# Performance work log

Measured on AMD Instinct MI355X. Metric: run time of the kernel, lower is better.

## Reference

```python
import jax, jax.numpy as jnp
import numpy as np

B, S, D_MODEL, H = 2, 2048, 1024, 16
DK = D_MODEL // H
THETA = 10000.0


def setup_inputs() -> dict:
    key = jax.random.key(0)
    ks = jax.random.split(key, 5)
    scale = 0.02  # keep logits in a numerically sane range
    return {
        "x": jax.random.normal(ks[0], (B, S, D_MODEL), jnp.float32),
        "Q_weight": jax.random.normal(ks[1], (D_MODEL, D_MODEL), jnp.float32) * scale,
        "K_weight": jax.random.normal(ks[2], (D_MODEL, D_MODEL), jnp.float32) * scale,
        "V_weight": jax.random.normal(ks[3], (D_MODEL, D_MODEL), jnp.float32) * scale,
        "O_weight": jax.random.normal(ks[4], (D_MODEL, D_MODEL), jnp.float32) * scale,
        "token_positions": jnp.arange(S, dtype=jnp.int32),
    }


def _rope(x, token_positions, theta, d_k):
    # x: [..., seq, d_k]; rotate interleaved even/odd pairs
    inv_freq = 1.0 / theta ** (jnp.arange(0, d_k, 2, dtype=jnp.float32) / d_k)
    ang = token_positions.astype(jnp.float32)[:, None] * inv_freq  # [S, d_k/2]
    cos, sin = jnp.cos(ang), jnp.sin(ang)
    x0, x1 = x[..., 0::2], x[..., 1::2]
    y0 = x0 * cos - x1 * sin
    y1 = x0 * sin + x1 * cos
    return jnp.stack([y0, y1], axis=-1).reshape(x.shape)


def _mhsa(x, Qw, Kw, Vw, Ow, token_positions):
    b, s, d = x.shape
    qw = Qw.reshape(H, DK, d)
    kw = Kw.reshape(H, DK, d)
    vw = Vw.reshape(H, DK, d)
    q = jnp.einsum('hki,bsi->bhsk', qw, x)
    k = jnp.einsum('hki,bsi->bhsk', kw, x)
    v = jnp.einsum('hvi,bsi->bhsv', vw, x)
    q = _rope(q, token_positions, THETA, DK)
    k = _rope(k, token_positions, THETA, DK)
    scores = jnp.einsum('bhnd,bhmd->bhnm', q, k) / jnp.sqrt(jnp.float32(DK))
    causal = jnp.tril(jnp.ones((s, s), dtype=bool))
    scores = jnp.where(causal, scores, -jnp.inf)
    attn = jax.nn.softmax(scores, axis=-1)
    o = jnp.einsum('bhnm,bhmv->bhnv', attn, v)  # [B,H,S,DV]
    o = jnp.transpose(o, (0, 2, 1, 3)).reshape(b, s, H * DK)
    return jnp.einsum('dv,bsv->bsd', Ow, o)


def reference(x, Q_weight, K_weight, V_weight, O_weight, token_positions):
    return _mhsa(x, Q_weight, K_weight, V_weight, O_weight, token_positions)
```

## Files before the change

kernel.cpp:

```cpp
#include <hip/hip_runtime.h>

#define NB 2
#define NS 2048
#define NDM 1024
#define NH 16
#define NDK 64

typedef unsigned int u32;
typedef u32 u32x4 __attribute__((ext_vector_type(4)));
typedef float f32x4 __attribute__((ext_vector_type(4)));
typedef float f32x2 __attribute__((ext_vector_type(2)));
typedef __bf16 bf16x8 __attribute__((ext_vector_type(8)));
typedef __bf16 bf16x4 __attribute__((ext_vector_type(4)));
typedef __bf16 bf16x2 __attribute__((ext_vector_type(2)));

#define QSCALE 0.18033688011112042f
#define EXP2F(x) __builtin_amdgcn_exp2f(x)

__device__ __forceinline__ void gload_lds16(const __bf16* g, __bf16* l) {
    __builtin_amdgcn_global_load_lds(
        (const __attribute__((address_space(1))) unsigned int*)(g),
        (__attribute__((address_space(3))) unsigned int*)(l), 16, 0, 0);
}

__global__ __launch_bounds__(256) void cvt_all(const float* __restrict__ x,
                                               const float* __restrict__ qw,
                                               const float* __restrict__ kw,
                                               const float* __restrict__ vw,
                                               const float* __restrict__ ow,
                                               const int* __restrict__ tp,
                                               __bf16* __restrict__ xb,
                                               __bf16* __restrict__ wqkv,
                                               __bf16* __restrict__ owb,
                                               float* __restrict__ tbl) {
    const int i = blockIdx.x * 256 + threadIdx.x;
    if (i >= 2097152) {
        const int it = i - 2097152;
        if (it < NS * 32) {
            const int s = it >> 5, jj = it & 31;
            const float pos = (float)tp[s];
            const float inv = exp2f(-0.41524101186092f * (float)jj);
            const float ang = pos * inv;
            float sn, cs;
            sincosf(ang, &sn, &cs);
            f32x2 o; o[0] = cs; o[1] = sn;
            *(f32x2*)&tbl[(size_t)it * 2] = o;
        }
        return;
    }
    const float* src;
    __bf16* dst;
    if (i < 1048576) {
        src = x + (size_t)i * 4;
        dst = xb + (size_t)i * 4;
    } else {
        const int j = i - 1048576;
        const int seg = j >> 18;
        const int off = j & 0x3FFFF;
        src = ((seg == 0) ? qw : (seg == 1) ? kw : (seg == 2) ? vw : ow) + (size_t)off * 4;
        if (seg <= 1) {
            const int row = off >> 8;
            const int c4 = off & 255;
            const int h = row >> 6, fr = row & 63;
            const int pr = (fr >> 1) | ((fr & 1) << 5);
            dst = wqkv + (((size_t)(seg << 10) + h * 64 + pr) << 10) + (size_t)c4 * 4;
        } else {
            dst = ((seg == 3) ? owb : wqkv + (size_t)seg * 1048576) + (size_t)off * 4;
        }
    }
    f32x4 v = *(const f32x4*)src;
    bf16x4 o;
    o[0] = (__bf16)v[0]; o[1] = (__bf16)v[1]; o[2] = (__bf16)v[2]; o[3] = (__bf16)v[3];
    *(bf16x4*)dst = o;
}

__global__ __launch_bounds__(256) void gemm_qkv128(const __bf16* __restrict__ A,
                                                   const __bf16* __restrict__ Bt,
                                                   const float* __restrict__ tbl,
                                                   __bf16* __restrict__ Qr,
                                                   __bf16* __restrict__ Kr,
                                                   __bf16* __restrict__ Vt) {
    __shared__ __bf16 As[2][128 * 64];
    __shared__ __bf16 Bs[2][128 * 64];
    const int K = 1024, lda = 1024, ldb = 1024;
    const int tid = threadIdx.x;
    const int lane = tid & 63, w = tid >> 6;
    const int wr = w >> 1, wc = w & 1;
    const int l15 = lane & 15, lg = lane >> 4;
    const int m0 = blockIdx.y * 128, n0 = blockIdx.x * 128;
    const int crow = lane >> 3;
    const int csw = ((lane & 7) ^ crow) * 8;

    f32x4 acc[4][4];
    const f32x4 z = {0.f, 0.f, 0.f, 0.f};
#pragma unroll
    for (int i = 0; i < 4; ++i)
#pragma unroll
        for (int jx = 0; jx < 4; ++jx) acc[i][jx] = z;

    auto stage = [&](int buf, int k0) {
#pragma unroll
        for (int ch = 0; ch < 4; ++ch) {
            const int cid = w * 4 + ch;
            const int ra = cid * 8 + crow;
            gload_lds16(&A[(size_t)(m0 + ra) * lda + k0 + csw], &As[buf][cid * 512]);
            gload_lds16(&Bt[(size_t)(n0 + ra) * ldb + k0 + csw], &Bs[buf][cid * 512]);
        }
    };

    stage(0, 0);
    int cur = 0;
    for (int k0 = 0; k0 < K; k0 += 64) {
        if (k0 + 64 < K) {
            stage(cur ^ 1, k0 + 64);
            asm volatile("s_waitcnt vmcnt(8)" ::: "memory");
        } else {
            asm volatile("s_waitcnt vmcnt(0)" ::: "memory");
        }
        __builtin_amdgcn_s_barrier();
        __builtin_amdgcn_sched_barrier(0);
#pragma unroll
        for (int kc = 0; kc < 2; ++kc) {
            bf16x8 af[4], bfv[4];
#pragma unroll
            for (int i = 0; i < 4; ++i) {
                const int ra = wr * 64 + i * 16 + l15;
                const int rb = wc * 64 + i * 16 + l15;
                af[i]  = *(const bf16x8*)&As[cur][ra * 64 + ((kc * 32 + lg * 8) ^ ((ra & 7) << 3))];
                bfv[i] = *(const bf16x8*)&Bs[cur][rb * 64 + ((kc * 32 + lg * 8) ^ ((rb & 7) << 3))];
            }
#pragma unroll
            for (int sm = 0; sm < 4; ++sm)
#pragma unroll
                for (int sn = 0; sn < 4; ++sn)
                    acc[sm][sn] = __builtin_amdgcn_mfma_f32_16x16x32_bf16(af[sm], bfv[sn], acc[sm][sn], 0, 0, 0);
        }
        asm volatile("s_waitcnt lgkmcnt(0)" ::: "memory");
        __builtin_amdgcn_s_barrier();
        __builtin_amdgcn_sched_barrier(0);
        cur ^= 1;
    }
    if (n0 < 2048) {
        __bf16* dst = (n0 < 1024) ? Qr : Kr;
        const float scale = (n0 < 1024) ? QSCALE : 1.0f;
        const int h = ((n0 & 1023) + wc * 64) >> 6;
#pragma unroll
        for (int sm = 0; sm < 4; ++sm)
#pragma unroll
            for (int j = 0; j < 4; ++j) {
                const int row = m0 + wr * 64 + sm * 16 + lg * 4 + j;
                const int b = row >> 11, s = row & (NS - 1);
                const size_t base = ((size_t)(b * NH + h) * NS + s) * 64;
#pragma unroll
                for (int pp = 0; pp < 2; ++pp) {
                    const int jj = pp * 16 + l15;
                    f32x2 cssn = *(const f32x2*)&tbl[((size_t)s * 32 + jj) * 2];
                    const float e  = acc[sm][pp][j];
                    const float od = acc[sm][pp + 2][j];
                    bf16x2 ov;
                    ov[0] = (__bf16)((e * cssn[0] - od * cssn[1]) * scale);
                    ov[1] = (__bf16)((e * cssn[1] + od * cssn[0]) * scale);
                    *(bf16x2*)&dst[base + 2 * jj] = ov;
                }
            }
    } else {
#pragma unroll
        for (int sm = 0; sm < 4; ++sm)
#pragma unroll
            for (int sn = 0; sn < 4; ++sn) {
                const int col = (n0 - 2048) + wc * 64 + sn * 16 + l15;
                const int h = col >> 6, d = col & 63;
                const int row = m0 + wr * 64 + sm * 16 + lg * 4;
                const int b = row >> 11, s = row & (NS - 1);
                bf16x4 ov;
#pragma unroll
                for (int j = 0; j < 4; ++j) ov[j] = (__bf16)acc[sm][sn][j];
                *(bf16x4*)&Vt[((size_t)(b * NH + h) * 64 + d) * NS + s] = ov;
            }
    }
}

template <typename TOUT>
__global__ __launch_bounds__(256) void gemm_bt128(const __bf16* __restrict__ A,
                                                  const __bf16* __restrict__ Bt,
                                                  TOUT* __restrict__ C,
                                                  int K, int lda, int ldb, int ldc) {
    __shared__ __bf16 As[2][128 * 64];
    __shared__ __bf16 Bs[2][128 * 64];
    const int tid = threadIdx.x;
    const int lane = tid & 63, w = tid >> 6;
    const int wr = w >> 1, wc = w & 1;
    const int l15 = lane & 15, lg = lane >> 4;
    const int m0 = blockIdx.y * 128, n0 = blockIdx.x * 128;
    const int crow = lane >> 3;
    const int csw = ((lane & 7) ^ crow) * 8;

    f32x4 acc[4][4];
    const f32x4 z = {0.f, 0.f, 0.f, 0.f};
#pragma unroll
    for (int i = 0; i < 4; ++i)
#pragma unroll
        for (int jx = 0; jx < 4; ++jx) acc[i][jx] = z;

    auto stage = [&](int buf, int k0) {
#pragma unroll
        for (int ch = 0; ch < 4; ++ch) {
            const int cid = w * 4 + ch;
            const int ra = cid * 8 + crow;
            gload_lds16(&A[(size_t)(m0 + ra) * lda + k0 + csw], &As[buf][cid * 512]);
            gload_lds16(&Bt[(size_t)(n0 + ra) * ldb + k0 + csw], &Bs[buf][cid * 512]);
        }
    };

    stage(0, 0);
    int cur = 0;
    for (int k0 = 0; k0 < K; k0 += 64) {
        if (k0 + 64 < K) {
            stage(cur ^ 1, k0 + 64);
            asm volatile("s_waitcnt vmcnt(8)" ::: "memory");
        } else {
            asm volatile("s_waitcnt vmcnt(0)" ::: "memory");
        }
        __builtin_amdgcn_s_barrier();
        __builtin_amdgcn_sched_barrier(0);
#pragma unroll
        for (int kc = 0; kc < 2; ++kc) {
            bf16x8 af[4], bfv[4];
#pragma unroll
            for (int i = 0; i < 4; ++i) {
                const int ra = wr * 64 + i * 16 + l15;
                const int rb = wc * 64 + i * 16 + l15;
                af[i]  = *(const bf16x8*)&As[cur][ra * 64 + ((kc * 32 + lg * 8) ^ ((ra & 7) << 3))];
                bfv[i] = *(const bf16x8*)&Bs[cur][rb * 64 + ((kc * 32 + lg * 8) ^ ((rb & 7) << 3))];
            }
#pragma unroll
            for (int sm = 0; sm < 4; ++sm)
#pragma unroll
                for (int sn = 0; sn < 4; ++sn)
                    acc[sm][sn] = __builtin_amdgcn_mfma_f32_16x16x32_bf16(af[sm], bfv[sn], acc[sm][sn], 0, 0, 0);
        }
        asm volatile("s_waitcnt lgkmcnt(0)" ::: "memory");
        __builtin_amdgcn_s_barrier();
        __builtin_amdgcn_sched_barrier(0);
        cur ^= 1;
    }
#pragma unroll
    for (int sm = 0; sm < 4; ++sm)
#pragma unroll
        for (int sn = 0; sn < 4; ++sn)
#pragma unroll
            for (int j = 0; j < 4; ++j) {
                const int row = m0 + wr * 64 + sm * 16 + lg * 4 + j;
                const int col = n0 + wc * 64 + sn * 16 + l15;
                C[(size_t)row * ldc + col] = (TOUT)acc[sm][sn][j];
            }
}

__device__ __forceinline__ int kperm(int rt) {
    const int ct = rt >> 4, rr = rt & 15;
    return ((rr >> 2) << 3) + ((ct >> 1) << 5) + ((ct & 1) << 2) + (rr & 3);
}

__global__ __launch_bounds__(256) void attn5(const __bf16* __restrict__ Qr,
                                             const __bf16* __restrict__ Kr,
                                             const __bf16* __restrict__ Vt,
                                             __bf16* __restrict__ O) {
    const int lid = blockIdx.x;
    const int xcd = lid & 7;
    const int g = lid >> 3;
    const int bh = xcd * 4 + (g & 3);
    const int pr = g >> 2;
    const int p = (pr < 8) ? (pr * 2) : (31 - 2 * pr);
    const int b = bh >> 4, h = bh & 15;
    const int tid = threadIdx.x;
    const int w = tid >> 6, lane = tid & 63;
    const int l15 = lane & 15, lg = lane >> 4;
    const __bf16* Qb = Qr + (size_t)bh * NS * 64;
    const __bf16* Kb = Kr + (size_t)bh * NS * 64;
    const __bf16* Vb = Vt + (size_t)bh * 64 * NS;

    __shared__ __bf16 Ks[2][64 * 64];
    __shared__ __bf16 Vs[2][64 * 64];

    const int rbv[2] = {p * 64 + w * 16, (31 - p) * 64 + w * 16};

    bf16x8 qf[2][2];
#pragma unroll
    for (int rs = 0; rs < 2; ++rs)
#pragma unroll
        for (int kc = 0; kc < 2; ++kc)
            qf[rs][kc] = *(const bf16x8*)(Qb + (size_t)(rbv[rs] + l15) * 64 + kc * 32 + lg * 8);

    f32x4 oacc[2][4];
    const f32x4 z = {0.f, 0.f, 0.f, 0.f};
#pragma unroll
    for (int rs = 0; rs < 2; ++rs)
#pragma unroll
        for (int ct = 0; ct < 4; ++ct) oacc[rs][ct] = z;
    float lsum[2] = {0.f, 0.f};

    const int crow = lane >> 3;
    const int cswz = ((lane & 7) ^ crow) * 8;

#pragma unroll
    for (int pp = 0; pp < 2; ++pp) {
        const int ch = w + pp * 4;
        const int rt = ch * 8 + crow;
        gload_lds16(Kb + (size_t)kperm(rt) * 64 + cswz, &Ks[0][ch * 512]);
        gload_lds16(Vb + (size_t)rt * NS + 0 + cswz, &Vs[0][ch * 512]);
    }
    __syncthreads();

    const int nt = 32 - p;
    for (int t = 0; t < nt; ++t) {
        const int cur = t & 1;
        const int kv0 = t << 6;
        if (t + 1 < nt) {
            const int kv1 = kv0 + 64;
#pragma unroll
            for (int pp = 0; pp < 2; ++pp) {
                const int ch = w + pp * 4;
                const int rt = ch * 8 + crow;
                gload_lds16(Kb + (size_t)(kv1 + kperm(rt)) * 64 + cswz, &Ks[cur ^ 1][ch * 512]);
                gload_lds16(Vb + (size_t)rt * NS + kv1 + cswz, &Vs[cur ^ 1][ch * 512]);
            }
        }
        bool act[2];
        act[0] = (kv0 <= rbv[0] + 15);
        act[1] = true;
        f32x4 sc[2][4];
#pragma unroll
        for (int rs = 0; rs < 2; ++rs)
            if (act[rs])
#pragma unroll
                for (int ct = 0; ct < 4; ++ct) sc[rs][ct] = z;
#pragma unroll
        for (int kc = 0; kc < 2; ++kc) {
            bf16x8 kf[4];
#pragma unroll
            for (int ct = 0; ct < 4; ++ct) {
                const int rt = ct * 16 + l15;
                kf[ct] = *(const bf16x8*)&Ks[cur][rt * 64 + ((kc * 32 + lg * 8) ^ ((rt & 7) << 3))];
            }
#pragma unroll
            for (int rs = 0; rs < 2; ++rs)
                if (act[rs])
#pragma unroll
                    for (int ct = 0; ct < 4; ++ct)
                        sc[rs][ct] = __builtin_amdgcn_mfma_f32_16x16x32_bf16(kf[ct], qf[rs][kc], sc[rs][ct], 0, 0, 0);
        }
        bf16x8 pb[2][2];
#pragma unroll
        for (int rs = 0; rs < 2; ++rs) {
            if (!act[rs]) continue;
            const int rbase = rbv[rs];
            const int qrow = rbase + l15;
            const bool needmask = (kv0 + 63 > rbase);
            if (needmask) {
#pragma unroll
                for (int ct = 0; ct < 4; ++ct)
#pragma unroll
                    for (int j = 0; j < 4; ++j) {
                        const int kvg = kv0 + ((ct >> 1) << 5) + lg * 8 + ((ct & 1) << 2) + j;
                        if (kvg > qrow) sc[rs][ct][j] = -1e30f;
                    }
            }
            float ps = 0.f;
#pragma unroll
            for (int ct = 0; ct < 4; ++ct)
#pragma unroll
                for (int j = 0; j < 4; ++j) {
                    const float e = EXP2F(sc[rs][ct][j]);
                    sc[rs][ct][j] = e;
                    ps += e;
                }
            lsum[rs] += ps;
#pragma unroll
            for (int kc = 0; kc < 2; ++kc) {
                bf16x8 pk;
                pk[0] = (__bf16)sc[rs][2 * kc][0];     pk[1] = (__bf16)sc[rs][2 * kc][1];
                pk[2] = (__bf16)sc[rs][2 * kc][2];     pk[3] = (__bf16)sc[rs][2 * kc][3];
                pk[4] = (__bf16)sc[rs][2 * kc + 1][0]; pk[5] = (__bf16)sc[rs][2 * kc + 1][1];
                pk[6] = (__bf16)sc[rs][2 * kc + 1][2]; pk[7] = (__bf16)sc[rs][2 * kc + 1][3];
                pb[rs][kc] = pk;
            }
        }
#pragma unroll
        for (int kc = 0; kc < 2; ++kc) {
            bf16x8 vf[4];
#pragma unroll
            for (int ct = 0; ct < 4; ++ct) {
                const int rt = ct * 16 + l15;
                vf[ct] = *(const bf16x8*)&Vs[cur][rt * 64 + ((kc * 32 + lg * 8) ^ ((rt & 7) << 3))];
            }
#pragma unroll
            for (int rs = 0; rs < 2; ++rs) {
                if (!act[rs]) continue;
#pragma unroll
                for (int ct = 0; ct < 4; ++ct)
                    oacc[rs][ct] = __builtin_amdgcn_mfma_f32_16x16x32_bf16(vf[ct], pb[rs][kc], oacc[rs][ct], 0, 0, 0);
            }
        }
        __syncthreads();
    }
#pragma unroll
    for (int rs = 0; rs < 2; ++rs) {
        float tot = lsum[rs];
        tot += __shfl_xor(tot, 16, 64);
        tot += __shfl_xor(tot, 32, 64);
        const float rl = 1.0f / tot;
        const size_t rowoff = (size_t)(b * NS + rbv[rs] + l15) * NDM + h * 64 + lg * 4;
#pragma unroll
        for (int ct = 0; ct < 4; ++ct) {
            bf16x4 ov;
#pragma unroll
            for (int j = 0; j < 4; ++j) ov[j] = (__bf16)(oacc[rs][ct][j] * rl);
            *(bf16x4*)&O[rowoff + ct * 16] = ov;
        }
    }
}

extern "C" void kernel_launch(void* const* d_in, const int* in_sizes, int n_in,
                              void* d_out, int out_size, void* d_ws, size_t ws_size,
                              hipStream_t stream) {
    const float* x  = (const float*)d_in[0];
    const float* Qw = (const float*)d_in[1];
    const float* Kw = (const float*)d_in[2];
    const float* Vw = (const float*)d_in[3];
    const float* Ow = (const float*)d_in[4];
    const int*   tp = (const int*)d_in[5];
    float* out = (float*)d_out;

    char* ws = (char*)d_ws;
    size_t off = 0;
    auto alloc = [&](size_t bytes) -> void* {
        void* p = ws + off;
        off += (bytes + 255) & ~(size_t)255;
        return p;
    };
    __bf16* xb   = (__bf16*)alloc((size_t)4096 * 1024 * 2);
    __bf16* wqkv = (__bf16*)alloc((size_t)3072 * 1024 * 2);
    __bf16* owb  = (__bf16*)alloc((size_t)1024 * 1024 * 2);
    __bf16* qr   = (__bf16*)alloc((size_t)32 * 2048 * 64 * 2);
    __bf16* kr   = (__bf16*)alloc((size_t)32 * 2048 * 64 * 2);
    __bf16* vt   = (__bf16*)alloc((size_t)32 * 64 * 2048 * 2);
    __bf16* ob   = (__bf16*)alloc((size_t)4096 * 1024 * 2);
    float*  tbl  = (float*)alloc((size_t)NS * 32 * 2 * 4);

    cvt_all<<<8448, 256, 0, stream>>>(x, Qw, Kw, Vw, Ow, tp, xb, wqkv, owb, tbl);

    gemm_qkv128<<<dim3(3072 / 128, 4096 / 128), 256, 0, stream>>>(xb, wqkv, tbl, qr, kr, vt);
    attn5<<<dim3(512), 256, 0, stream>>>(qr, kr, vt, ob);
    gemm_bt128<float><<<dim3(1024 / 128, 4096 / 128), 256, 0, stream>>>(
        ob, owb, out, 1024, 1024, 1024, 1024);
}
```

Before: 112.6 us.

## Split paired causal query tiles into one tile per block, longest first

The attention kernel previously paired a short and a long causal query tile in each block (512 blocks) so that every block did equal work. It now gives each block a single 64-row query tile (1024 blocks), ordered so the tiles with the most KV steps launch first, and applies the causal mask only on the final diagonal tile. This raises block count and cuts register use per block, which may improve occupancy and simplify the inner loop. In exchange, each K/V tile loaded into LDS now serves half as many query rows, so K/V traffic roughly doubles, and load balance now depends on the longest-first ordering.

```diff
diff --git a/kernel.cpp b/kernel.cpp
--- a/kernel.cpp
+++ b/kernel.cpp
@@ -261,7 +261,7 @@
     return ((rr >> 2) << 3) + ((ct >> 1) << 5) + ((ct & 1) << 2) + (rr & 3);
 }
 
-__global__ __launch_bounds__(256) void attn5(const __bf16* __restrict__ Qr,
+__global__ __launch_bounds__(256) void attn9(const __bf16* __restrict__ Qr,
                                              const __bf16* __restrict__ Kr,
                                              const __bf16* __restrict__ Vt,
                                              __bf16* __restrict__ O) {
@@ -269,8 +269,8 @@
     const int xcd = lid & 7;
     const int g = lid >> 3;
     const int bh = xcd * 4 + (g & 3);
-    const int pr = g >> 2;
-    const int p = (pr < 8) ? (pr * 2) : (31 - 2 * pr);
+    const int ti = 31 - (g >> 2);
+    const int q0 = ti * 64;
     const int b = bh >> 4, h = bh & 15;
     const int tid = threadIdx.x;
     const int w = tid >> 6, lane = tid & 63;
@@ -282,22 +282,18 @@
     __shared__ __bf16 Ks[2][64 * 64];
     __shared__ __bf16 Vs[2][64 * 64];
 
-    const int rbv[2] = {p * 64 + w * 16, (31 - p) * 64 + w * 16};
-
-    bf16x8 qf[2][2];
-#pragma unroll
-    for (int rs = 0; rs < 2; ++rs)
-#pragma unroll
-        for (int kc = 0; kc < 2; ++kc)
-            qf[rs][kc] = *(const bf16x8*)(Qb + (size_t)(rbv[rs] + l15) * 64 + kc * 32 + lg * 8);
-
-    f32x4 oacc[2][4];
+    const int rb = q0 + w * 16;
+
+    bf16x8 qf[2];
+#pragma unroll
+    for (int kc = 0; kc < 2; ++kc)
+        qf[kc] = *(const bf16x8*)(Qb + (size_t)(rb + l15) * 64 + kc * 32 + lg * 8);
+
+    f32x4 oacc[4];
     const f32x4 z = {0.f, 0.f, 0.f, 0.f};
 #pragma unroll
-    for (int rs = 0; rs < 2; ++rs)
-#pragma unroll
-        for (int ct = 0; ct < 4; ++ct) oacc[rs][ct] = z;
-    float lsum[2] = {0.f, 0.f};
+    for (int ct = 0; ct < 4; ++ct) oacc[ct] = z;
+    float lsum = 0.f;
 
     const int crow = lane >> 3;
     const int cswz = ((lane & 7) ^ crow) * 8;
@@ -311,7 +307,7 @@
     }
     __syncthreads();
 
-    const int nt = 32 - p;
+    const int nt = ti + 1;
     for (int t = 0; t < nt; ++t) {
         const int cur = t & 1;
         const int kv0 = t << 6;
@@ -325,15 +321,9 @@
                 gload_lds16(Vb + (size_t)rt * NS + kv1 + cswz, &Vs[cur ^ 1][ch * 512]);
             }
         }
-        bool act[2];
-        act[0] = (kv0 <= rbv[0] + 15);
-        act[1] = true;
-        f32x4 sc[2][4];
-#pragma unroll
-        for (int rs = 0; rs < 2; ++rs)
-            if (act[rs])
-#pragma unroll
-                for (int ct = 0; ct < 4; ++ct) sc[rs][ct] = z;
+        f32x4 sc[4];
+#pragma unroll
+        for (int ct = 0; ct < 4; ++ct) sc[ct] = z;
 #pragma unroll
         for (int kc = 0; kc < 2; ++kc) {
             bf16x8 kf[4];
@@ -343,47 +333,38 @@
                 kf[ct] = *(const bf16x8*)&Ks[cur][rt * 64 + ((kc * 32 + lg * 8) ^ ((rt & 7) << 3))];
             }
 #pragma unroll
-            for (int rs = 0; rs < 2; ++rs)
-                if (act[rs])
-#pragma unroll
-                    for (int ct = 0; ct < 4; ++ct)
-                        sc[rs][ct] = __builtin_amdgcn_mfma_f32_16x16x32_bf16(kf[ct], qf[rs][kc], sc[rs][ct], 0, 0, 0);
-        }
-        bf16x8 pb[2][2];
-#pragma unroll
-        for (int rs = 0; rs < 2; ++rs) {
-            if (!act[rs]) continue;
-            const int rbase = rbv[rs];
-            const int qrow = rbase + l15;
-            const bool needmask = (kv0 + 63 > rbase);
-            if (needmask) {
-#pragma unroll
-                for (int ct = 0; ct < 4; ++ct)
-#pragma unroll
-                    for (int j = 0; j < 4; ++j) {
-                        const int kvg = kv0 + ((ct >> 1) << 5) + lg * 8 + ((ct & 1) << 2) + j;
-                        if (kvg > qrow) sc[rs][ct][j] = -1e30f;
-                    }
-            }
-            float ps = 0.f;
-#pragma unroll
             for (int ct = 0; ct < 4; ++ct)
+                sc[ct] = __builtin_amdgcn_mfma_f32_16x16x32_bf16(kf[ct], qf[kc], sc[ct], 0, 0, 0);
+        }
+        const int qrow = rb + l15;
+        if (t == nt - 1) {
+#pragma unroll
+            for (int ct = 0; ct < 4; ++ct)
 #pragma unroll
                 for (int j = 0; j < 4; ++j) {
-                    const float e = EXP2F(sc[rs][ct][j]);
-                    sc[rs][ct][j] = e;
-                    ps += e;
+                    const int kvg = kv0 + ((ct >> 1) << 5) + lg * 8 + ((ct & 1) << 2) + j;
+                    if (kvg > qrow) sc[ct][j] = -1e30f;
                 }
-            lsum[rs] += ps;
-#pragma unroll
-            for (int kc = 0; kc < 2; ++kc) {
-                bf16x8 pk;
-                pk[0] = (__bf16)sc[rs][2 * kc][0];     pk[1] = (__bf16)sc[rs][2 * kc][1];
-                pk[2] = (__bf16)sc[rs][2 * kc][2];     pk[3] = (__bf16)sc[rs][2 * kc][3];
-                pk[4] = (__bf16)sc[rs][2 * kc + 1][0]; pk[5] = (__bf16)sc[rs][2 * kc + 1][1];
-                pk[6] = (__bf16)sc[rs][2 * kc + 1][2]; pk[7] = (__bf16)sc[rs][2 * kc + 1][3];
-                pb[rs][kc] = pk;
-            }
+        }
+        float ps = 0.f;
+#pragma unroll
+        for (int ct = 0; ct < 4; ++ct)
+#pragma unroll
+            for (int j = 0; j < 4; ++j) {
+                const float e = EXP2F(sc[ct][j]);
+                sc[ct][j] = e;
+                ps += e;
+            }
+        lsum += ps;
+        bf16x8 pb[2];
+#pragma unroll
+        for (int kc = 0; kc < 2; ++kc) {
+            bf16x8 pk;
+            pk[0] = (__bf16)sc[2 * kc][0];     pk[1] = (__bf16)sc[2 * kc][1];
+            pk[2] = (__bf16)sc[2 * kc][2];     pk[3] = (__bf16)sc[2 * kc][3];
+            pk[4] = (__bf16)sc[2 * kc + 1][0]; pk[5] = (__bf16)sc[2 * kc + 1][1];
+            pk[6] = (__bf16)sc[2 * kc + 1][2]; pk[7] = (__bf16)sc[2 * kc + 1][3];
+            pb[kc] = pk;
         }
 #pragma unroll
         for (int kc = 0; kc < 2; ++kc) {
@@ -394,29 +375,22 @@
                 vf[ct] = *(const bf16x8*)&Vs[cur][rt * 64 + ((kc * 32 + lg * 8) ^ ((rt & 7) << 3))];
             }
 #pragma unroll
-            for (int rs = 0; rs < 2; ++rs) {
-                if (!act[rs]) continue;
-#pragma unroll
-                for (int ct = 0; ct < 4; ++ct)
-                    oacc[rs][ct] = __builtin_amdgcn_mfma_f32_16x16x32_bf16(vf[ct], pb[rs][kc], oacc[rs][ct], 0, 0, 0);
-            }
+            for (int ct = 0; ct < 4; ++ct)
+                oacc[ct] = __builtin_amdgcn_mfma_f32_16x16x32_bf16(vf[ct], pb[kc], oacc[ct], 0, 0, 0);
         }
         __syncthreads();
     }
-#pragma unroll
-    for (int rs = 0; rs < 2; ++rs) {
-        float tot = lsum[rs];
-        tot += __shfl_xor(tot, 16, 64);
-        tot += __shfl_xor(tot, 32, 64);
-        const float rl = 1.0f / tot;
-        const size_t rowoff = (size_t)(b * NS + rbv[rs] + l15) * NDM + h * 64 + lg * 4;
-#pragma unroll
-        for (int ct = 0; ct < 4; ++ct) {
-            bf16x4 ov;
-#pragma unroll
-            for (int j = 0; j < 4; ++j) ov[j] = (__bf16)(oacc[rs][ct][j] * rl);
-            *(bf16x4*)&O[rowoff + ct * 16] = ov;
-        }
+    float tot = lsum;
+    tot += __shfl_xor(tot, 16, 64);
+    tot += __shfl_xor(tot, 32, 64);
+    const float rl = 1.0f / tot;
+    const size_t rowoff = (size_t)(b * NS + rb + l15) * NDM + h * 64 + lg * 4;
+#pragma unroll
+    for (int ct = 0; ct < 4; ++ct) {
+        bf16x4 ov;
+#pragma unroll
+        for (int j = 0; j < 4; ++j) ov[j] = (__bf16)(oacc[ct][j] * rl);
+        *(bf16x4*)&O[rowoff + ct * 16] = ov;
     }
 }
 
@@ -450,7 +424,7 @@
     cvt_all<<<8448, 256, 0, stream>>>(x, Qw, Kw, Vw, Ow, tp, xb, wqkv, owb, tbl);
 
     gemm_qkv128<<<dim3(3072 / 128, 4096 / 128), 256, 0, stream>>>(xb, wqkv, tbl, qr, kr, vt);
-    attn5<<<dim3(512), 256, 0, stream>>>(qr, kr, vt, ob);
+    attn9<<<dim3(1024), 256, 0, stream>>>(qr, kr, vt, ob);
     gemm_bt128<float><<<dim3(1024 / 128, 4096 / 128), 256, 0, stream>>>(
         ob, owb, out, 1024, 1024, 1024, 1024);
 }
```

Measured after the change: 108.8 us, median of 3. -3.4%, faster.
